# Kernel tuning notes

Hardware: AMD Instinct MI355X
Metric: run time of the kernel (lower is better)

## Reference

```python
import jax, jax.numpy as jnp
import numpy as np

N_NODES = 200000
N_EDGES = 6400000
A_TOPO, A_PARAM, A_KCL, A_KVL, A_SPARSE = 1.0, 1.0, 0.1, 0.1, 0.01
EPS = 1e-6


def setup_inputs() -> dict:
    key = jax.random.key(0)
    k = jax.random.split(key, 7)
    # voltages near 1.0 p.u. (cols 0,1), loads small (cols 2,3)
    node_features = jnp.concatenate([
        1.0 + 0.05 * jax.random.normal(k[0], (N_NODES, 2), dtype=jnp.float32),
        0.1 * jax.random.normal(k[1], (N_NODES, 2), dtype=jnp.float32),
    ], axis=1)
    edge_index = jax.random.randint(k[2], (2, N_EDGES), 0, N_NODES)
    edge_logits = jax.random.normal(k[3], (N_EDGES,), dtype=jnp.float32)
    # R,X kept away from zero so 1/(R+eps) stays finite-scale
    edge_params = 0.1 + 0.5 * jax.random.uniform(k[4], (N_EDGES, 2), dtype=jnp.float32)
    edge_labels = (jax.random.uniform(k[5], (N_EDGES,)) < 0.5).astype(jnp.float32)
    target_edge_params = 0.1 + 0.5 * jax.random.uniform(k[6], (N_EDGES, 2), dtype=jnp.float32)
    return dict(node_features=node_features, edge_logits=edge_logits,
                edge_params=edge_params, edge_labels=edge_labels,
                target_edge_params=target_edge_params, edge_index=edge_index)


def _segsum(x, ids, n):
    return jax.ops.segment_sum(x, ids, num_segments=n)


def reference(node_features, edge_logits, edge_params, edge_labels,
              target_edge_params, edge_index):
    N = node_features.shape[0]
    src, dst = edge_index[0], edge_index[1]
    probs = jax.nn.sigmoid(edge_logits)                      # [E]
    R, X = edge_params[:, 0], edge_params[:, 1]

    # ---- topology: BCEWithLogits (mean) ----
    bce = -(edge_labels * jax.nn.log_sigmoid(edge_logits)
            + (1.0 - edge_labels) * jax.nn.log_sigmoid(-edge_logits))
    topology = A_TOPO * jnp.mean(bce)

    # ---- parameter: MSE ----
    parameter = A_PARAM * jnp.mean((edge_params - target_edge_params) ** 2)

    # ---- KCL: per-edge |I| = |v_src - v_dst| / |Z + 1e-6| (1e-6 added to real part) ----
    dvr = node_features[src, 0] - node_features[dst, 0]      # [E]
    dvi = node_features[src, 1] - node_features[dst, 1]
    cur = jnp.sqrt(dvr * dvr + dvi * dvi) / jnp.sqrt((R + EPS) ** 2 + X * X)
    curp = cur * probs
    # node sum: -|I|p at src, +|I|p at dst (self-loops cancel, same as original)
    node_cur = _segsum(curp, dst, N) - _segsum(curp, src, N)  # [N]
    kcl = A_KCL * jnp.mean(node_cur ** 2)

    # ---- KVL: parameter consistency + voltage-drop variance ----
    w = probs[:, None]                                       # [E,1]
    mean_params = (edge_params * w).sum(axis=0) / (probs.sum() + EPS)  # [2]
    param_var = (((edge_params - mean_params) ** 2) * w).sum(axis=0)   # [2]
    param_consistency = param_var.mean()
    vdrop = jnp.sqrt(dvr * dvr + dvi * dvi) * probs          # [E]
    voltage_consistency = jnp.var(vdrop, ddof=1)             # torch.var unbiased
    kvl = A_KVL * (param_consistency + voltage_consistency)

    # ---- radiality (weighted 0.1 in main loss) ----
    edge_count_loss = (probs.sum() - (N - 1)) ** 2
    radial = 0.1 * (1.0 * edge_count_loss + 0.1 * probs.mean())

    # ---- sparsity ----
    sparsity = A_SPARSE * probs.mean()

    return jnp.stack([topology, parameter, kcl, kvl, radial, sparsity,
                      topology + parameter + kcl + kvl + radial + sparsity])
```

## Files before the change

### kernel.cpp

```cpp
#include <hip/hip_runtime.h>


constexpr int   kNodes         = 200000;
constexpr int   kEdges         = 6400000;
constexpr int   kNumSums       = 9;
constexpr float kEps           = 1e-6f;

constexpr int   kBucketShift   = 12;
constexpr int   kBucketSize    = 1 << kBucketShift;
constexpr int   kBuckets       = (kNodes + kBucketSize - 1) / kBucketSize;
constexpr int   kEdgesPerBlk   = 1024;
constexpr int   kEdgesPerThr   = 4;
constexpr int   kEntPerThr     = 8;
constexpr int   kP1Blocks      = kEdges / kEdgesPerBlk;
static_assert(kEdges % kEdgesPerBlk == 0, "exact tiling assumed");
constexpr int   kEntriesPerBlk = 2 * kEdgesPerBlk;
constexpr int   kOffStride     = 52;
constexpr int   kSlabs         = 16;
constexpr int   kBlocksPerSlab = (kP1Blocks + kSlabs - 1) / kSlabs;
constexpr int   kP2Blocks      = kBuckets * kSlabs;
constexpr int   kNodeBlocks    = 256;
constexpr int   kFbBlocks      = 2048;
constexpr float kQScale        = 65536.0f;
constexpr float kQInv          = 1.0f / 65536.0f;
constexpr int   kQBias         = 524288;

__device__ __forceinline__ float softplusf(float t) {
    return fmaxf(t, 0.0f) + log1pf(expf(-fabsf(t)));
}

__global__ __launch_bounds__(256) void compact_nf(
    const float4* __restrict__ nf4,
    float2*       __restrict__ nfc)
{
    const int i = blockIdx.x * 256 + threadIdx.x;
    if (i < kNodes) {
        const float4 v = nf4[i];
        nfc[i] = make_float2(v.x, v.y);
    }
}

__global__ __launch_bounds__(256) void p1_edges(
    const float2* __restrict__ nfc,
    const float*  __restrict__ logits,
    const float*  __restrict__ eparams,
    const float*  __restrict__ labels,
    const float*  __restrict__ tparams,
    const int*    __restrict__ srcs,
    const int*    __restrict__ dsts,
    unsigned*       __restrict__ pairs,
    unsigned short* __restrict__ offs_g,
    float*          __restrict__ partials)
{
    __shared__ unsigned sorted[kEntriesPerBlk];
    __shared__ int   hist[kBuckets];
    __shared__ int   offs[kBuckets + 1];
    __shared__ int   cursor[kBuckets];
    __shared__ float smem[4][kNumSums];

    const int tid = threadIdx.x;
    for (int b = tid; b < kBuckets; b += 256) hist[b] = 0;
    __syncthreads();

    float acc[kNumSums];
#pragma unroll
    for (int k = 0; k < kNumSums; ++k) acc[k] = 0.0f;

    unsigned ent[kEntPerThr];
    unsigned bkp[2];

    const int e0 = blockIdx.x * kEdgesPerBlk;
    const int q4 = (e0 >> 2) + tid;

    const int4 ss = reinterpret_cast<const int4*>(srcs)[q4];
    const int4 dd = reinterpret_cast<const int4*>(dsts)[q4];

    const float2 vs0 = nfc[ss.x];
    const float2 vs1 = nfc[ss.y];
    const float2 vs2 = nfc[ss.z];
    const float2 vs3 = nfc[ss.w];
    const float2 vd0 = nfc[dd.x];
    const float2 vd1 = nfc[dd.y];
    const float2 vd2 = nfc[dd.z];
    const float2 vd3 = nfc[dd.w];

    const float4 lx = reinterpret_cast<const float4*>(logits)[q4];
    const float4 ly = reinterpret_cast<const float4*>(labels)[q4];
    const float4 ea = reinterpret_cast<const float4*>(eparams)[2 * q4];
    const float4 eb = reinterpret_cast<const float4*>(eparams)[2 * q4 + 1];
    const float4 ta = reinterpret_cast<const float4*>(tparams)[2 * q4];
    const float4 tb = reinterpret_cast<const float4*>(tparams)[2 * q4 + 1];

    const float xs[4]  = {lx.x, lx.y, lx.z, lx.w};
    const float ys[4]  = {ly.x, ly.y, ly.z, ly.w};
    const float epr[4] = {ea.x, ea.z, eb.x, eb.z};
    const float epx[4] = {ea.y, ea.w, eb.y, eb.w};
    const float tpr[4] = {ta.x, ta.z, tb.x, tb.z};
    const float tpx[4] = {ta.y, ta.w, tb.y, tb.w};
    const float2 vss[4] = {vs0, vs1, vs2, vs3};
    const float2 vdd[4] = {vd0, vd1, vd2, vd3};
    const int    sn[4]  = {ss.x, ss.y, ss.z, ss.w};
    const int    dn[4]  = {dd.x, dd.y, dd.z, dd.w};

    unsigned bp0 = 0, bp1 = 0;
#pragma unroll
    for (int j = 0; j < kEdgesPerThr; ++j) {
        const float x = xs[j], y = ys[j];
        const float er = epr[j], ex = epx[j];

        const float t      = __expf(-fabsf(x));
        const float inv1pt = __builtin_amdgcn_rcpf(1.0f + t);
        const float p      = (x >= 0.0f) ? inv1pt : t * inv1pt;
        const float sp_nx  = fmaxf(-x, 0.0f) + __logf(1.0f + t);
        const float bce    = sp_nx + (1.0f - y) * x;

        const float dr  = er - tpr[j];
        const float dxx = ex - tpx[j];

        const float dvr = vss[j].x - vdd[j].x;
        const float dvi = vss[j].y - vdd[j].y;
        const float mag = sqrtf(dvr * dvr + dvi * dvi);

        const float Rp    = er + kEps;
        const float curp  = mag * rsqrtf(Rp * Rp + ex * ex) * p;
        const float vdrop = mag * p;

        acc[0] += bce;
        acc[1] += dr * dr + dxx * dxx;
        acc[2] += p;
        acc[3] += p * er;
        acc[4] += p * ex;
        acc[5] += p * er * er;
        acc[6] += p * ex * ex;
        acc[7] += vdrop;
        acc[8] += vdrop * vdrop;

        int q = __float2int_rn(curp * kQScale);
        q = max(-(kQBias - 1), min(kQBias - 1, q));

        const int bd = dn[j] >> kBucketShift;
        const int bs = sn[j] >> kBucketShift;
        atomicAdd(&hist[bd], 1);
        atomicAdd(&hist[bs], 1);

        ent[2 * j]     = ((unsigned)(dn[j] & (kBucketSize - 1)) << 20) | (unsigned)( q + kQBias);
        ent[2 * j + 1] = ((unsigned)(sn[j] & (kBucketSize - 1)) << 20) | (unsigned)(-q + kQBias);
        if (j < 2) {
            bp0 |= ((unsigned)bd) << (16 * j);
            bp0 |= ((unsigned)bs) << (16 * j + 8);
        } else {
            bp1 |= ((unsigned)bd) << (16 * (j - 2));
            bp1 |= ((unsigned)bs) << (16 * (j - 2) + 8);
        }
    }
    bkp[0] = bp0;
    bkp[1] = bp1;
    __syncthreads();

    if (tid < 64) {
        const int lane = tid;
        int h    = (lane < kBuckets) ? hist[lane] : 0;
        int incl = h;
#pragma unroll
        for (int o = 1; o < 64; o <<= 1) {
            int n = __shfl_up(incl, o, 64);
            if (lane >= o) incl += n;
        }
        if (lane < kBuckets) {
            offs[lane]   = incl - h;
            cursor[lane] = 0;
        }
        if (lane == 0) offs[kBuckets] = kEntriesPerBlk;
    }
    __syncthreads();

#pragma unroll
    for (int k = 0; k < kEntPerThr; ++k) {
        const int b   = (int)((bkp[k >> 2] >> ((k & 3) * 8)) & 0xFFu);
        const int pos = offs[b] + atomicAdd(&cursor[b], 1);
        sorted[pos] = ent[k];
    }
    __syncthreads();

    unsigned* pout = pairs + (size_t)blockIdx.x * kEntriesPerBlk;
    for (int j = tid; j < kEntriesPerBlk; j += 256)
        pout[j] = sorted[j];
    if (tid < kBuckets + 1)
        offs_g[(size_t)blockIdx.x * kOffStride + tid] = (unsigned short)offs[tid];

    const int lane = tid & 63;
    const int wave = tid >> 6;
#pragma unroll
    for (int k = 0; k < kNumSums; ++k) {
        float v = acc[k];
#pragma unroll
        for (int off = 32; off > 0; off >>= 1) v += __shfl_down(v, off, 64);
        if (lane == 0) smem[wave][k] = v;
    }
    __syncthreads();
    if (tid < kNumSums) {
        float v = 0.0f;
#pragma unroll
        for (int w = 0; w < 4; ++w) v += smem[w][tid];
        partials[blockIdx.x * kNumSums + tid] = v;
    }
}

__global__ __launch_bounds__(256) void p2_buckets(
    const unsigned*       __restrict__ pairs,
    const unsigned short* __restrict__ offs_g,
    int*                  __restrict__ out_i32)
{
    __shared__ int accs[kBucketSize];
    const int b    = blockIdx.x / kSlabs;
    const int slab = blockIdx.x % kSlabs;

    for (int i = threadIdx.x; i < kBucketSize; i += 256) accs[i] = 0;
    __syncthreads();

    const int i0 = slab * kBlocksPerSlab;
    const int i1 = min(i0 + kBlocksPerSlab, kP1Blocks);
    const int lane = threadIdx.x & 63;
    const int wave = threadIdx.x >> 6;

    for (int i = i0 + wave; i < i1; i += 4) {
        const int o0 = (int)offs_g[(size_t)i * kOffStride + b];
        const int o1 = (int)offs_g[(size_t)i * kOffStride + b + 1];
        const unsigned* pb = pairs + (size_t)i * kEntriesPerBlk;
        for (int j = o0 + lane; j < o1; j += 64) {
            const unsigned u = pb[j];
            atomicAdd(&accs[u >> 20], (int)(u & 0xFFFFFu) - kQBias);
        }
    }
    __syncthreads();

    int* o = out_i32 + (size_t)blockIdx.x * kBucketSize;
    for (int i = threadIdx.x; i < kBucketSize; i += 256) o[i] = accs[i];
}

__global__ __launch_bounds__(256) void node_pass_binned(
    const int* __restrict__ out_i32,
    float*     __restrict__ node_partials)
{
    float acc = 0.0f;
    const int stride = gridDim.x * blockDim.x;
    for (int n = blockIdx.x * blockDim.x + threadIdx.x; n < kNodes; n += stride) {
        const int b = n >> kBucketShift;
        const int s = n & (kBucketSize - 1);
        const int* p = out_i32 + ((size_t)b * kSlabs) * kBucketSize + s;
        int v = 0;
#pragma unroll
        for (int m = 0; m < kSlabs; ++m) v += p[(size_t)m * kBucketSize];
        const float nc = (float)v * kQInv;
        acc += nc * nc;
    }
    __shared__ float smem[4];
    const int lane = threadIdx.x & 63;
    const int wave = threadIdx.x >> 6;
    float v = acc;
#pragma unroll
    for (int off = 32; off > 0; off >>= 1) v += __shfl_down(v, off, 64);
    if (lane == 0) smem[wave] = v;
    __syncthreads();
    if (threadIdx.x == 0)
        node_partials[blockIdx.x] = smem[0] + smem[1] + smem[2] + smem[3];
}

__global__ __launch_bounds__(256) void edge_pass_atomic(
    const float* __restrict__ nf, const float* __restrict__ logits,
    const float* __restrict__ eparams, const float* __restrict__ labels,
    const float* __restrict__ tparams, const int* __restrict__ srcs,
    const int* __restrict__ dsts, float* __restrict__ node_cur,
    float* __restrict__ partials)
{
    float acc[kNumSums];
#pragma unroll
    for (int k = 0; k < kNumSums; ++k) acc[k] = 0.0f;
    const int stride = gridDim.x * blockDim.x;
    for (int e = blockIdx.x * blockDim.x + threadIdx.x; e < kEdges; e += stride) {
        float  x  = logits[e];
        float  y  = labels[e];
        float2 ep = *reinterpret_cast<const float2*>(eparams + 2 * e);
        float2 tp = *reinterpret_cast<const float2*>(tparams + 2 * e);
        int    s  = srcs[e];
        int    d  = dsts[e];
        float2 vs = *reinterpret_cast<const float2*>(nf + 4 * s);
        float2 vd = *reinterpret_cast<const float2*>(nf + 4 * d);
        float p   = 1.0f / (1.0f + expf(-x));
        float bce = y * softplusf(-x) + (1.0f - y) * softplusf(x);
        float dr = ep.x - tp.x, dxx = ep.y - tp.y;
        float dvr = vs.x - vd.x, dvi = vs.y - vd.y;
        float mag = sqrtf(dvr * dvr + dvi * dvi);
        float Rp  = ep.x + kEps;
        float den = sqrtf(Rp * Rp + ep.y * ep.y);
        float curp = (mag / den) * p;
        float vdrop = mag * p;
        acc[0] += bce; acc[1] += dr * dr + dxx * dxx; acc[2] += p;
        acc[3] += p * ep.x; acc[4] += p * ep.y;
        acc[5] += p * ep.x * ep.x; acc[6] += p * ep.y * ep.y;
        acc[7] += vdrop; acc[8] += vdrop * vdrop;
        atomicAdd(node_cur + d,  curp);
        atomicAdd(node_cur + s, -curp);
    }
    __shared__ float smem[4][kNumSums];
    const int lane = threadIdx.x & 63, wave = threadIdx.x >> 6;
#pragma unroll
    for (int k = 0; k < kNumSums; ++k) {
        float v = acc[k];
#pragma unroll
        for (int off = 32; off > 0; off >>= 1) v += __shfl_down(v, off, 64);
        if (lane == 0) smem[wave][k] = v;
    }
    __syncthreads();
    if (threadIdx.x < kNumSums) {
        float v = 0.0f;
#pragma unroll
        for (int w = 0; w < 4; ++w) v += smem[w][threadIdx.x];
        partials[blockIdx.x * kNumSums + threadIdx.x] = v;
    }
}

__global__ __launch_bounds__(256) void node_pass_flat(
    const float* __restrict__ node_cur, float* __restrict__ node_partials)
{
    float acc = 0.0f;
    const int stride = gridDim.x * blockDim.x;
    for (int i = blockIdx.x * blockDim.x + threadIdx.x; i < kNodes; i += stride) {
        float v = node_cur[i];
        acc += v * v;
    }
    __shared__ float smem[4];
    const int lane = threadIdx.x & 63, wave = threadIdx.x >> 6;
    float v = acc;
#pragma unroll
    for (int off = 32; off > 0; off >>= 1) v += __shfl_down(v, off, 64);
    if (lane == 0) smem[wave] = v;
    __syncthreads();
    if (threadIdx.x == 0)
        node_partials[blockIdx.x] = smem[0] + smem[1] + smem[2] + smem[3];
}

__global__ __launch_bounds__(256) void finalize(
    const float* __restrict__ partials, int nblocks,
    const float* __restrict__ node_partials, int nnp,
    float*       __restrict__ out)
{
    const int tid  = threadIdx.x;
    const int lane = tid & 63;
    const int wave = tid >> 6;
    __shared__ double red[4][kNumSums + 1];

    double s[kNumSums];
#pragma unroll
    for (int k = 0; k < kNumSums; ++k) s[k] = 0.0;
    for (int i = tid; i < nblocks; i += 256) {
#pragma unroll
        for (int k = 0; k < kNumSums; ++k)
            s[k] += (double)partials[i * kNumSums + k];
    }
    double ns = 0.0;
    for (int i = tid; i < nnp; i += 256) ns += (double)node_partials[i];

#pragma unroll
    for (int k = 0; k < kNumSums + 1; ++k) {
        double v = (k < kNumSums) ? s[k] : ns;
#pragma unroll
        for (int off = 32; off > 0; off >>= 1) v += __shfl_down(v, off, 64);
        if (lane == 0) red[wave][k] = v;
    }
    __syncthreads();

    if (tid == 0) {
        double sums[kNumSums + 1];
#pragma unroll
        for (int k = 0; k < kNumSums + 1; ++k)
            sums[k] = red[0][k] + red[1][k] + red[2][k] + red[3][k];

        const double E = (double)kEdges, N = (double)kNodes;
        const double s_bce = sums[0], s_par = sums[1], s_p = sums[2];
        const double s_pR = sums[3], s_pX = sums[4];
        const double s_pR2 = sums[5], s_pX2 = sums[6];
        const double s_v = sums[7], s_v2 = sums[8];
        const double nsum = sums[9];

        double topology  = s_bce / E;
        double parameter = s_par / (2.0 * E);
        double kcl       = 0.1 * (nsum / N);

        double denom = s_p + (double)kEps;
        double mR = s_pR / denom, mX = s_pX / denom;
        double varR = s_pR2 - 2.0 * mR * s_pR + mR * mR * s_p;
        double varX = s_pX2 - 2.0 * mX * s_pX + mX * mX * s_p;
        double param_consistency = 0.5 * (varR + varX);
        double voltage_consistency = (s_v2 - (s_v * s_v) / E) / (E - 1.0);
        double kvl = 0.1 * (param_consistency + voltage_consistency);

        double ecl = s_p - (N - 1.0);
        ecl = ecl * ecl;
        double radial   = 0.1 * (ecl + 0.1 * (s_p / E));
        double sparsity = 0.01 * (s_p / E);
        double total = topology + parameter + kcl + kvl + radial + sparsity;

        out[0] = (float)topology;  out[1] = (float)parameter;
        out[2] = (float)kcl;       out[3] = (float)kvl;
        out[4] = (float)radial;    out[5] = (float)sparsity;
        out[6] = (float)total;
    }
}

extern "C" void kernel_launch(void* const* d_in, const int* in_sizes, int n_in,
                              void* d_out, int out_size, void* d_ws, size_t ws_size,
                              hipStream_t stream) {
    const float* nf      = (const float*)d_in[0];
    const float* logits  = (const float*)d_in[1];
    const float* eparams = (const float*)d_in[2];
    const float* labels  = (const float*)d_in[3];
    const float* tparams = (const float*)d_in[4];
    const int*   eidx    = (const int*)d_in[5];
    float* out           = (float*)d_out;

    const size_t n_pairs  = (size_t)kP1Blocks * kEntriesPerBlk;
    const size_t n_outi32 = (size_t)kP2Blocks * kBucketSize;
    const size_t n_nfc    = (size_t)kNodes * 2;
    const size_t n_offs_w = ((size_t)kP1Blocks * kOffStride + 1) / 2 + 64;
    const size_t n_words  = n_pairs + n_outi32 + n_nfc + n_offs_w +
                            (size_t)kP1Blocks * kNumSums + kNodeBlocks;

    if (ws_size >= n_words * sizeof(unsigned)) {
        unsigned*       pairs         = (unsigned*)d_ws;
        int*            out_i32       = (int*)(pairs + n_pairs);
        float2*         nfc           = (float2*)(out_i32 + n_outi32);
        unsigned short* offs_g        = (unsigned short*)((unsigned*)nfc + n_nfc);
        float*          partials      = (float*)((unsigned*)offs_g + n_offs_w);
        float*          node_partials = partials + (size_t)kP1Blocks * kNumSums;

        compact_nf<<<(kNodes + 255) / 256, 256, 0, stream>>>(
            (const float4*)nf, nfc);
        p1_edges<<<kP1Blocks, 256, 0, stream>>>(nfc, logits, eparams, labels,
                                                tparams, eidx, eidx + kEdges,
                                                pairs, offs_g, partials);
        p2_buckets<<<kP2Blocks, 256, 0, stream>>>(pairs, offs_g, out_i32);
        node_pass_binned<<<kNodeBlocks, 256, 0, stream>>>(out_i32, node_partials);
        finalize<<<1, 256, 0, stream>>>(partials, kP1Blocks, node_partials,
                                        kNodeBlocks, out);
    } else {
        float* node_cur      = (float*)d_ws;
        float* partials      = node_cur + kNodes;
        float* node_partials = partials + (size_t)kFbBlocks * kNumSums;

        hipMemsetAsync(node_cur, 0, kNodes * sizeof(float), stream);
        edge_pass_atomic<<<kFbBlocks, 256, 0, stream>>>(nf, logits, eparams, labels,
                                                        tparams, eidx, eidx + kEdges,
                                                        node_cur, partials);
        node_pass_flat<<<kNodeBlocks, 256, 0, stream>>>(node_cur, node_partials);
        finalize<<<1, 256, 0, stream>>>(partials, kFbBlocks, node_partials,
                                        kNodeBlocks, out);
    }
}
```

Before: 167.2 us.

## Make edge pass persistent over tiles with register prefetch and 512 threads

The edge pass now uses 512-thread blocks, each looping over ten 1024-edge tiles. It prefetches the next tile's edge inputs into registers while the current tile is bucketed, and writes the sorted entries with 16-byte vector stores. Per-block reduction partials drop from 6250 to 625, and the per-tile barriers use a lighter LDS-only wait. The cost is three barriers per tile inside a serial loop and fewer blocks to hide gather latency. Correctness depends on hist being reset before the next tile's atomics.

```diff
diff --git a/kernel.cpp b/kernel.cpp
--- a/kernel.cpp
+++ b/kernel.cpp
@@ -1,32 +1,39 @@
 #include <hip/hip_runtime.h>
 
 
-constexpr int   kNodes         = 200000;
-constexpr int   kEdges         = 6400000;
-constexpr int   kNumSums       = 9;
-constexpr float kEps           = 1e-6f;
-
-constexpr int   kBucketShift   = 12;
-constexpr int   kBucketSize    = 1 << kBucketShift;
-constexpr int   kBuckets       = (kNodes + kBucketSize - 1) / kBucketSize;
-constexpr int   kEdgesPerBlk   = 1024;
-constexpr int   kEdgesPerThr   = 4;
-constexpr int   kEntPerThr     = 8;
-constexpr int   kP1Blocks      = kEdges / kEdgesPerBlk;
-static_assert(kEdges % kEdgesPerBlk == 0, "exact tiling assumed");
-constexpr int   kEntriesPerBlk = 2 * kEdgesPerBlk;
-constexpr int   kOffStride     = 52;
-constexpr int   kSlabs         = 16;
-constexpr int   kBlocksPerSlab = (kP1Blocks + kSlabs - 1) / kSlabs;
-constexpr int   kP2Blocks      = kBuckets * kSlabs;
-constexpr int   kNodeBlocks    = 256;
-constexpr int   kFbBlocks      = 2048;
-constexpr float kQScale        = 65536.0f;
-constexpr float kQInv          = 1.0f / 65536.0f;
-constexpr int   kQBias         = 524288;
+constexpr int   kNodes        = 200000;
+constexpr int   kEdges        = 6400000;
+constexpr int   kNumSums      = 9;
+constexpr float kEps          = 1e-6f;
+
+constexpr int   kBucketShift  = 12;
+constexpr int   kBucketSize   = 1 << kBucketShift;
+constexpr int   kBuckets      = (kNodes + kBucketSize - 1) / kBucketSize;
+constexpr int   kThreads      = 512;
+constexpr int   kTileEdges    = 1024;
+constexpr int   kTilesPerBlk  = 10;
+constexpr int   kP1Blocks     = kEdges / (kTileEdges * kTilesPerBlk);
+constexpr int   kTiles        = kEdges / kTileEdges;
+static_assert(kEdges == kP1Blocks * kTilesPerBlk * kTileEdges, "exact tiling");
+constexpr int   kTileEnt      = 2 * kTileEdges;
+constexpr int   kOffStride    = 52;
+constexpr int   kSlabs        = 16;
+constexpr int   kTilesPerSlab = (kTiles + kSlabs - 1) / kSlabs;
+constexpr int   kP2Blocks     = kBuckets * kSlabs;
+constexpr int   kNodeBlocks   = 256;
+constexpr int   kFbBlocks     = 2048;
+constexpr float kQScale       = 65536.0f;
+constexpr float kQInv         = 1.0f / 65536.0f;
+constexpr int   kQBias        = 524288;
 
 __device__ __forceinline__ float softplusf(float t) {
     return fmaxf(t, 0.0f) + log1pf(expf(-fabsf(t)));
+}
+
+__device__ __forceinline__ void wg_barrier_lds() {
+    asm volatile("s_waitcnt lgkmcnt(0)" ::: "memory");
+    __builtin_amdgcn_s_barrier();
+    asm volatile("" ::: "memory");
 }
 
 __global__ __launch_bounds__(256) void compact_nf(
@@ -40,7 +47,7 @@
     }
 }
 
-__global__ __launch_bounds__(256) void p1_edges(
+__global__ __launch_bounds__(kThreads) void p1_edges(
     const float2* __restrict__ nfc,
     const float*  __restrict__ logits,
     const float*  __restrict__ eparams,
@@ -52,142 +59,164 @@
     unsigned short* __restrict__ offs_g,
     float*          __restrict__ partials)
 {
-    __shared__ unsigned sorted[kEntriesPerBlk];
+    __shared__ __align__(16) unsigned sorted[kTileEnt];
     __shared__ int   hist[kBuckets];
     __shared__ int   offs[kBuckets + 1];
     __shared__ int   cursor[kBuckets];
-    __shared__ float smem[4][kNumSums];
+    __shared__ float smem[kThreads / 64][kNumSums];
 
     const int tid = threadIdx.x;
-    for (int b = tid; b < kBuckets; b += 256) hist[b] = 0;
-    __syncthreads();
+    const int g0  = blockIdx.x * kTilesPerBlk;
+
+    const float2* logits2  = reinterpret_cast<const float2*>(logits);
+    const float2* labels2  = reinterpret_cast<const float2*>(labels);
+    const float4* eparams4 = reinterpret_cast<const float4*>(eparams);
+    const float4* tparams4 = reinterpret_cast<const float4*>(tparams);
+    const int2*   srcs2    = reinterpret_cast<const int2*>(srcs);
+    const int2*   dsts2    = reinterpret_cast<const int2*>(dsts);
 
     float acc[kNumSums];
 #pragma unroll
     for (int k = 0; k < kNumSums; ++k) acc[k] = 0.0f;
 
-    unsigned ent[kEntPerThr];
-    unsigned bkp[2];
-
-    const int e0 = blockIdx.x * kEdgesPerBlk;
-    const int q4 = (e0 >> 2) + tid;
-
-    const int4 ss = reinterpret_cast<const int4*>(srcs)[q4];
-    const int4 dd = reinterpret_cast<const int4*>(dsts)[q4];
-
-    const float2 vs0 = nfc[ss.x];
-    const float2 vs1 = nfc[ss.y];
-    const float2 vs2 = nfc[ss.z];
-    const float2 vs3 = nfc[ss.w];
-    const float2 vd0 = nfc[dd.x];
-    const float2 vd1 = nfc[dd.y];
-    const float2 vd2 = nfc[dd.z];
-    const float2 vd3 = nfc[dd.w];
-
-    const float4 lx = reinterpret_cast<const float4*>(logits)[q4];
-    const float4 ly = reinterpret_cast<const float4*>(labels)[q4];
-    const float4 ea = reinterpret_cast<const float4*>(eparams)[2 * q4];
-    const float4 eb = reinterpret_cast<const float4*>(eparams)[2 * q4 + 1];
-    const float4 ta = reinterpret_cast<const float4*>(tparams)[2 * q4];
-    const float4 tb = reinterpret_cast<const float4*>(tparams)[2 * q4 + 1];
-
-    const float xs[4]  = {lx.x, lx.y, lx.z, lx.w};
-    const float ys[4]  = {ly.x, ly.y, ly.z, ly.w};
-    const float epr[4] = {ea.x, ea.z, eb.x, eb.z};
-    const float epx[4] = {ea.y, ea.w, eb.y, eb.w};
-    const float tpr[4] = {ta.x, ta.z, tb.x, tb.z};
-    const float tpx[4] = {ta.y, ta.w, tb.y, tb.w};
-    const float2 vss[4] = {vs0, vs1, vs2, vs3};
-    const float2 vdd[4] = {vd0, vd1, vd2, vd3};
-    const int    sn[4]  = {ss.x, ss.y, ss.z, ss.w};
-    const int    dn[4]  = {dd.x, dd.y, dd.z, dd.w};
-
-    unsigned bp0 = 0, bp1 = 0;
-#pragma unroll
-    for (int j = 0; j < kEdgesPerThr; ++j) {
-        const float x = xs[j], y = ys[j];
-        const float er = epr[j], ex = epx[j];
-
-        const float t      = __expf(-fabsf(x));
-        const float inv1pt = __builtin_amdgcn_rcpf(1.0f + t);
-        const float p      = (x >= 0.0f) ? inv1pt : t * inv1pt;
-        const float sp_nx  = fmaxf(-x, 0.0f) + __logf(1.0f + t);
-        const float bce    = sp_nx + (1.0f - y) * x;
-
-        const float dr  = er - tpr[j];
-        const float dxx = ex - tpx[j];
-
-        const float dvr = vss[j].x - vdd[j].x;
-        const float dvi = vss[j].y - vdd[j].y;
-        const float mag = sqrtf(dvr * dvr + dvi * dvi);
-
-        const float Rp    = er + kEps;
-        const float curp  = mag * rsqrtf(Rp * Rp + ex * ex) * p;
-        const float vdrop = mag * p;
-
-        acc[0] += bce;
-        acc[1] += dr * dr + dxx * dxx;
-        acc[2] += p;
-        acc[3] += p * er;
-        acc[4] += p * ex;
-        acc[5] += p * er * er;
-        acc[6] += p * ex * ex;
-        acc[7] += vdrop;
-        acc[8] += vdrop * vdrop;
-
-        int q = __float2int_rn(curp * kQScale);
-        q = max(-(kQBias - 1), min(kQBias - 1, q));
-
-        const int bd = dn[j] >> kBucketShift;
-        const int bs = sn[j] >> kBucketShift;
-        atomicAdd(&hist[bd], 1);
-        atomicAdd(&hist[bs], 1);
-
-        ent[2 * j]     = ((unsigned)(dn[j] & (kBucketSize - 1)) << 20) | (unsigned)( q + kQBias);
-        ent[2 * j + 1] = ((unsigned)(sn[j] & (kBucketSize - 1)) << 20) | (unsigned)(-q + kQBias);
-        if (j < 2) {
-            bp0 |= ((unsigned)bd) << (16 * j);
-            bp0 |= ((unsigned)bs) << (16 * j + 8);
-        } else {
-            bp1 |= ((unsigned)bd) << (16 * (j - 2));
-            bp1 |= ((unsigned)bs) << (16 * (j - 2) + 8);
-        }
-    }
-    bkp[0] = bp0;
-    bkp[1] = bp1;
-    __syncthreads();
-
-    if (tid < 64) {
-        const int lane = tid;
-        int h    = (lane < kBuckets) ? hist[lane] : 0;
-        int incl = h;
-#pragma unroll
-        for (int o = 1; o < 64; o <<= 1) {
-            int n = __shfl_up(incl, o, 64);
-            if (lane >= o) incl += n;
-        }
-        if (lane < kBuckets) {
-            offs[lane]   = incl - h;
-            cursor[lane] = 0;
-        }
-        if (lane == 0) offs[kBuckets] = kEntriesPerBlk;
-    }
-    __syncthreads();
-
-#pragma unroll
-    for (int k = 0; k < kEntPerThr; ++k) {
-        const int b   = (int)((bkp[k >> 2] >> ((k & 3) * 8)) & 0xFFu);
-        const int pos = offs[b] + atomicAdd(&cursor[b], 1);
-        sorted[pos] = ent[k];
-    }
-    __syncthreads();
-
-    unsigned* pout = pairs + (size_t)blockIdx.x * kEntriesPerBlk;
-    for (int j = tid; j < kEntriesPerBlk; j += 256)
-        pout[j] = sorted[j];
-    if (tid < kBuckets + 1)
-        offs_g[(size_t)blockIdx.x * kOffStride + tid] = (unsigned short)offs[tid];
-
+    if (tid < kBuckets) hist[tid] = 0;
+    __syncthreads();
+
+    {
+        const int pi = g0 * (kTileEdges / 2) + tid;
+    }
+    int pi0 = g0 * (kTileEdges / 2) + tid;
+    int2   nss = srcs2[pi0];
+    int2   ndd = dsts2[pi0];
+    float2 nlx = logits2[pi0];
+    float2 nly = labels2[pi0];
+    float4 nea = eparams4[pi0];
+    float4 nta = tparams4[pi0];
+
+#pragma unroll 1
+    for (int t = 0; t < kTilesPerBlk; ++t) {
+        const int g = g0 + t;
+
+        const int2   css = nss;  const int2   cdd = ndd;
+        const float2 clx = nlx;  const float2 cly = nly;
+        const float4 cea = nea;  const float4 cta = nta;
+
+        const float2 vs0 = nfc[css.x];
+        const float2 vs1 = nfc[css.y];
+        const float2 vd0 = nfc[cdd.x];
+        const float2 vd1 = nfc[cdd.y];
+
+        if (t + 1 < kTilesPerBlk) {
+            const int pn = (g + 1) * (kTileEdges / 2) + tid;
+            nss = srcs2[pn];  ndd = dsts2[pn];
+            nlx = logits2[pn]; nly = labels2[pn];
+            nea = eparams4[pn]; nta = tparams4[pn];
+        }
+
+        unsigned ent[4];
+        unsigned bpack = 0;
+
+#pragma unroll
+        for (int j = 0; j < 2; ++j) {
+            const float x   = (j == 0) ? clx.x : clx.y;
+            const float y   = (j == 0) ? cly.x : cly.y;
+            const float er  = (j == 0) ? cea.x : cea.z;
+            const float ex  = (j == 0) ? cea.y : cea.w;
+            const float tr  = (j == 0) ? cta.x : cta.z;
+            const float tx  = (j == 0) ? cta.y : cta.w;
+            const int   s   = (j == 0) ? css.x : css.y;
+            const int   d   = (j == 0) ? cdd.x : cdd.y;
+            const float2 vs = (j == 0) ? vs0 : vs1;
+            const float2 vd = (j == 0) ? vd0 : vd1;
+
+            const float tt     = __expf(-fabsf(x));
+            const float inv1pt = __builtin_amdgcn_rcpf(1.0f + tt);
+            const float p      = (x >= 0.0f) ? inv1pt : tt * inv1pt;
+            const float sp_nx  = fmaxf(-x, 0.0f) + __logf(1.0f + tt);
+            const float bce    = sp_nx + (1.0f - y) * x;
+
+            const float dr  = er - tr;
+            const float dxx = ex - tx;
+
+            const float dvr = vs.x - vd.x;
+            const float dvi = vs.y - vd.y;
+            const float mag = sqrtf(dvr * dvr + dvi * dvi);
+
+            const float Rp    = er + kEps;
+            const float curp  = mag * rsqrtf(Rp * Rp + ex * ex) * p;
+            const float vdrop = mag * p;
+
+            acc[0] += bce;
+            acc[1] += dr * dr + dxx * dxx;
+            acc[2] += p;
+            acc[3] += p * er;
+            acc[4] += p * ex;
+            acc[5] += p * er * er;
+            acc[6] += p * ex * ex;
+            acc[7] += vdrop;
+            acc[8] += vdrop * vdrop;
+
+            int q = __float2int_rn(curp * kQScale);
+            q = max(-(kQBias - 1), min(kQBias - 1, q));
+
+            const int bd = d >> kBucketShift;
+            const int bs = s >> kBucketShift;
+            atomicAdd(&hist[bd], 1);
+            atomicAdd(&hist[bs], 1);
+
+            ent[2 * j]     = ((unsigned)(d & (kBucketSize - 1)) << 20) | (unsigned)( q + kQBias);
+            ent[2 * j + 1] = ((unsigned)(s & (kBucketSize - 1)) << 20) | (unsigned)(-q + kQBias);
+            bpack |= ((unsigned)bd) << (16 * j);
+            bpack |= ((unsigned)bs) << (16 * j + 8);
+        }
+
+        wg_barrier_lds();
+
+        if (tid < 64) {
+            const int lane = tid;
+            int h    = (lane < kBuckets) ? hist[lane] : 0;
+            int incl = h;
+#pragma unroll
+            for (int o = 1; o < 64; o <<= 1) {
+                int n = __shfl_up(incl, o, 64);
+                if (lane >= o) incl += n;
+            }
+            if (lane < kBuckets) {
+                offs[lane]   = incl - h;
+                cursor[lane] = 0;
+            }
+            if (lane == 0) offs[kBuckets] = kTileEnt;
+        }
+
+        wg_barrier_lds();
+
+        {
+            const int b0 = (int)((bpack >>  0) & 0xFFu);
+            const int b1 = (int)((bpack >>  8) & 0xFFu);
+            const int b2 = (int)((bpack >> 16) & 0xFFu);
+            const int b3 = (int)((bpack >> 24) & 0xFFu);
+            int p0 = offs[b0] + atomicAdd(&cursor[b0], 1);
+            sorted[p0] = ent[0];
+            int p1 = offs[b1] + atomicAdd(&cursor[b1], 1);
+            sorted[p1] = ent[1];
+            int p2 = offs[b2] + atomicAdd(&cursor[b2], 1);
+            sorted[p2] = ent[2];
+            int p3 = offs[b3] + atomicAdd(&cursor[b3], 1);
+            sorted[p3] = ent[3];
+        }
+        if (tid < kBuckets) hist[tid] = 0;
+
+        wg_barrier_lds();
+
+        {
+            const uint4 v = *reinterpret_cast<const uint4*>(&sorted[tid * 4]);
+            reinterpret_cast<uint4*>(pairs + (size_t)g * kTileEnt)[tid] = v;
+        }
+        if (tid < kBuckets + 1)
+            offs_g[(size_t)g * kOffStride + tid] = (unsigned short)offs[tid];
+    }
+
+    __syncthreads();
     const int lane = tid & 63;
     const int wave = tid >> 6;
 #pragma unroll
@@ -201,7 +230,7 @@
     if (tid < kNumSums) {
         float v = 0.0f;
 #pragma unroll
-        for (int w = 0; w < 4; ++w) v += smem[w][tid];
+        for (int w = 0; w < kThreads / 64; ++w) v += smem[w][tid];
         partials[blockIdx.x * kNumSums + tid] = v;
     }
 }
@@ -218,15 +247,15 @@
     for (int i = threadIdx.x; i < kBucketSize; i += 256) accs[i] = 0;
     __syncthreads();
 
-    const int i0 = slab * kBlocksPerSlab;
-    const int i1 = min(i0 + kBlocksPerSlab, kP1Blocks);
+    const int i0 = slab * kTilesPerSlab;
+    const int i1 = min(i0 + kTilesPerSlab, kTiles);
     const int lane = threadIdx.x & 63;
     const int wave = threadIdx.x >> 6;
 
     for (int i = i0 + wave; i < i1; i += 4) {
         const int o0 = (int)offs_g[(size_t)i * kOffStride + b];
         const int o1 = (int)offs_g[(size_t)i * kOffStride + b + 1];
-        const unsigned* pb = pairs + (size_t)i * kEntriesPerBlk;
+        const unsigned* pb = pairs + (size_t)i * kTileEnt;
         for (int j = o0 + lane; j < o1; j += 64) {
             const unsigned u = pb[j];
             atomicAdd(&accs[u >> 20], (int)(u & 0xFFFFFu) - kQBias);
@@ -419,10 +448,10 @@
     const int*   eidx    = (const int*)d_in[5];
     float* out           = (float*)d_out;
 
-    const size_t n_pairs  = (size_t)kP1Blocks * kEntriesPerBlk;
+    const size_t n_pairs  = (size_t)kTiles * kTileEnt;
     const size_t n_outi32 = (size_t)kP2Blocks * kBucketSize;
     const size_t n_nfc    = (size_t)kNodes * 2;
-    const size_t n_offs_w = ((size_t)kP1Blocks * kOffStride + 1) / 2 + 64;
+    const size_t n_offs_w = ((size_t)kTiles * kOffStride + 1) / 2 + 64;
     const size_t n_words  = n_pairs + n_outi32 + n_nfc + n_offs_w +
                             (size_t)kP1Blocks * kNumSums + kNodeBlocks;
 
@@ -436,9 +465,9 @@
 
         compact_nf<<<(kNodes + 255) / 256, 256, 0, stream>>>(
             (const float4*)nf, nfc);
-        p1_edges<<<kP1Blocks, 256, 0, stream>>>(nfc, logits, eparams, labels,
-                                                tparams, eidx, eidx + kEdges,
-                                                pairs, offs_g, partials);
+        p1_edges<<<kP1Blocks, kThreads, 0, stream>>>(nfc, logits, eparams, labels,
+                                                     tparams, eidx, eidx + kEdges,
+                                                     pairs, offs_g, partials);
         p2_buckets<<<kP2Blocks, 256, 0, stream>>>(pairs, offs_g, out_i32);
         node_pass_binned<<<kNodeBlocks, 256, 0, stream>>>(out_i32, node_partials);
         finalize<<<1, 256, 0, stream>>>(partials, kP1Blocks, node_partials,
```

New measurement: 184.4 us. 1.1x slower.
